# Kernel optimization log

Hardware: AMD Instinct MI355X
Metric: run time of the kernel (lower is better)

The kernel has to match this reference:

```python
import jax, jax.numpy as jnp
import numpy as np

DEGREE = 7

def setup_inputs() -> dict:
    key = jax.random.key(0)
    k1, k2 = jax.random.split(key)
    input_dims, output_dims = 1024, 1024
    x = jax.random.normal(k1, (8192, input_dims), dtype=jnp.float32)
    std = 1.0 / (input_dims * (DEGREE + 1))
    lucas_coeffs = std * jax.random.normal(k2, (input_dims, output_dims, DEGREE + 1), dtype=jnp.float32)
    return {"x": x, "lucas_coeffs": lucas_coeffs}

def reference(x, lucas_coeffs):
    input_dims = lucas_coeffs.shape[0]
    x = x.reshape(-1, input_dims)
    x = jnp.tanh(x)
    # Lucas polynomial recurrence: L0=2, L1=x, L_i = x*L_{i-1} + L_{i-2}
    basis = [jnp.full_like(x, 2.0)]
    if DEGREE > 0:
        basis.append(x)
    for i in range(2, DEGREE + 1):
        basis.append(x * basis[-1] + basis[-2])
    lucas = jnp.stack(basis, axis=-1)  # [b, i, d]
    y = jnp.einsum('bid,iod->bo', lucas, lucas_coeffs)
    return y
```

## Files before the change

kernel.cpp:

```cpp
#include <hip/hip_runtime.h>
#include <hip/hip_bf16.h>


typedef __attribute__((ext_vector_type(8)))  short  short8;
typedef __attribute__((ext_vector_type(4)))  unsigned short ushort4v;
typedef __attribute__((ext_vector_type(8)))  unsigned short ushort8;
typedef __attribute__((ext_vector_type(4)))  float  float4v;
typedef __attribute__((ext_vector_type(4)))  unsigned int uint4v;

#define M_DIM 8192
#define I_DIM 1024
#define O_DIM 1024
#define K_DIM 8192
#define BM 128
#define BN 128
#define BK 64
#define KSPLIT 2
#define KHALF (K_DIM / KSPLIT)
#define NSTEP (KHALF / BK)

__device__ __forceinline__ unsigned short f2bf(float f) {
    unsigned int u = __float_as_uint(f);
    u += 0x7FFFu + ((u >> 16) & 1u);
    return (unsigned short)(u >> 16);
}

__global__ __launch_bounds__(256) void zero_kernel(float* __restrict__ p) {
    int idx = (blockIdx.x * 256 + threadIdx.x) * 4;
    const float4v z = {0.f, 0.f, 0.f, 0.f};
    *(float4v*)(p + idx) = z;
}

__global__ __launch_bounds__(256) void prep_kernel(const float* __restrict__ x,
                                                   const float* __restrict__ c,
                                                   unsigned short* __restrict__ T,
                                                   unsigned short* __restrict__ Bt) {
    int bid = blockIdx.x;
    const int tPart = (M_DIM * I_DIM) / (8 * 256);
    if (bid < tPart) {
        int idx = (bid * 256 + threadIdx.x) * 8;
        float4v v0 = *(const float4v*)(x + idx);
        float4v v1 = *(const float4v*)(x + idx + 4);
        unsigned short t[8];
        t[0] = f2bf(tanhf(v0[0])); t[1] = f2bf(tanhf(v0[1]));
        t[2] = f2bf(tanhf(v0[2])); t[3] = f2bf(tanhf(v0[3]));
        t[4] = f2bf(tanhf(v1[0])); t[5] = f2bf(tanhf(v1[1]));
        t[6] = f2bf(tanhf(v1[2])); t[7] = f2bf(tanhf(v1[3]));
        ushort8 o;
        #pragma unroll
        for (int p = 0; p < 4; ++p) { o[2 * p] = t[p]; o[2 * p + 1] = t[p + 4]; }
        *(ushort8*)(T + idx) = o;
    } else {
        int idx = (bid - tPart) * 256 + threadIdx.x;
        int i = idx >> 10;
        int o = idx & 1023;
        const float* src = c + (size_t)i * 8192 + o * 8;
        float4v lo = *(const float4v*)(src);
        float4v hi = *(const float4v*)(src + 4);
        ushort8 v;
        v[0] = f2bf(lo[0]); v[1] = f2bf(lo[1]); v[2] = f2bf(lo[2]); v[3] = f2bf(lo[3]);
        v[4] = f2bf(hi[0]); v[5] = f2bf(hi[1]); v[6] = f2bf(hi[2]); v[7] = f2bf(hi[3]);
        *(ushort8*)(Bt + (size_t)o * K_DIM + i * 8) = v;
    }
}

__device__ __forceinline__ short8 lucas_frag(unsigned int tb) {
    const float t = __uint_as_float(tb << 16);
    const float L2v = fmaf(t, t, 2.0f);
    const float L3v = fmaf(t, L2v, t);
    const float L4v = fmaf(t, L3v, L2v);
    const float L5v = fmaf(t, L4v, L3v);
    const float L6v = fmaf(t, L5v, L4v);
    const float L7v = fmaf(t, L6v, L5v);
    union { uint4v u; short8 s; } r;
#if __has_builtin(__builtin_amdgcn_cvt_pk_bf16_f32)
    {
        auto p0 = __builtin_amdgcn_cvt_pk_bf16_f32(2.0f, t);
        auto p1 = __builtin_amdgcn_cvt_pk_bf16_f32(L2v, L3v);
        auto p2 = __builtin_amdgcn_cvt_pk_bf16_f32(L4v, L5v);
        auto p3 = __builtin_amdgcn_cvt_pk_bf16_f32(L6v, L7v);
        __builtin_memcpy(&r.u[0], &p0, 4);
        __builtin_memcpy(&r.u[1], &p1, 4);
        __builtin_memcpy(&r.u[2], &p2, 4);
        __builtin_memcpy(&r.u[3], &p3, 4);
    }
#else
    {
        r.u[0] = 0x4000u | (tb << 16);
        r.u[1] = __builtin_amdgcn_perm(__float_as_uint(L3v), __float_as_uint(L2v), 0x07060302);
        r.u[2] = __builtin_amdgcn_perm(__float_as_uint(L5v), __float_as_uint(L4v), 0x07060302);
        r.u[3] = __builtin_amdgcn_perm(__float_as_uint(L7v), __float_as_uint(L6v), 0x07060302);
    }
#endif
    return r.s;
}

__global__ __launch_bounds__(256, 4) void gemm_kernel(const unsigned short* __restrict__ T,
                                                      const unsigned short* __restrict__ Bt,
                                                      float* __restrict__ out) {
    __shared__ unsigned short Bs[2][BN * BK];
    __shared__ unsigned short Ts[2][BM * 8];

    const int tid  = threadIdx.x;
    const int lane = tid & 63;
    const int wave = tid >> 6;
    const int n0 = blockIdx.x * BN;
    const int m0 = blockIdx.y * BM;
    const int k0 = blockIdx.z * KHALF;

    const int wm0  = (wave >> 1) * 64;
    const int wn0  = (wave & 1) * 64;
    const int l16  = lane & 15;
    const int quad = lane >> 4;

    const int srow   = lane >> 3;
    const int il     = lane & 7;
    const int gchunk = il ^ srow;

    float4v acc[4][4];
    const float4v zero = {0.f, 0.f, 0.f, 0.f};
    #pragma unroll
    for (int a = 0; a < 4; ++a)
        #pragma unroll
        for (int b = 0; b < 4; ++b) acc[a][b] = zero;

    #pragma unroll
    for (int r = 0; r < 4; ++r) {
        const int rowb = r * 32 + wave * 8;
        const unsigned short* gB = Bt + (size_t)(n0 + rowb + srow) * K_DIM + k0 + gchunk * 8;
        __builtin_amdgcn_global_load_lds(
            (const __attribute__((address_space(1))) unsigned int*)gB,
            (__attribute__((address_space(3))) unsigned int*)&Bs[0][rowb * BK], 16, 0, 0);
    }
    if (wave < 2) {
        const unsigned short* gT = T + (size_t)(m0 + wave * 64 + lane) * I_DIM + k0 / 8;
        __builtin_amdgcn_global_load_lds(
            (const __attribute__((address_space(1))) unsigned int*)gT,
            (__attribute__((address_space(3))) unsigned int*)&Ts[0][wave * 64 * 8], 16, 0, 0);
    }
    __syncthreads();

    int cur = 0;
    for (int s = 0; s < NSTEP; ++s) {
        const int nxt = cur ^ 1;

        if (s + 1 < NSTEP) {
            const int kt = k0 + (s + 1) * BK;
            #pragma unroll
            for (int r = 0; r < 4; ++r) {
                const int rowb = r * 32 + wave * 8;
                const unsigned short* gB = Bt + (size_t)(n0 + rowb + srow) * K_DIM + kt + gchunk * 8;
                __builtin_amdgcn_global_load_lds(
                    (const __attribute__((address_space(1))) unsigned int*)gB,
                    (__attribute__((address_space(3))) unsigned int*)&Bs[nxt][rowb * BK], 16, 0, 0);
            }
            if (wave < 2) {
                const unsigned short* gT = T + (size_t)(m0 + wave * 64 + lane) * I_DIM + kt / 8;
                __builtin_amdgcn_global_load_lds(
                    (const __attribute__((address_space(1))) unsigned int*)gT,
                    (__attribute__((address_space(3))) unsigned int*)&Ts[nxt][wave * 64 * 8], 16, 0, 0);
            }
        }

        unsigned int tw[4];
        #pragma unroll
        for (int tt = 0; tt < 4; ++tt)
            tw[tt] = *(const unsigned int*)&Ts[cur][(wm0 + tt * 16 + l16) * 8 + quad * 2];

        #pragma unroll
        for (int k2 = 0; k2 < 2; ++k2) {
            short8 bfr[4];
            #pragma unroll
            for (int tn = 0; tn < 4; ++tn) {
                const int brow = wn0 + tn * 16 + l16;
                bfr[tn] = *(const short8*)&Bs[cur][brow * BK + (((k2 * 4 + quad) ^ (l16 & 7)) * 8)];
            }
            #pragma unroll
            for (int tt = 0; tt < 4; ++tt) {
                const short8 af = lucas_frag(k2 ? (tw[tt] >> 16) : (tw[tt] & 0xffffu));
                #pragma unroll
                for (int tn = 0; tn < 4; ++tn)
                    acc[tt][tn] = __builtin_amdgcn_mfma_f32_16x16x32_bf16(
                        af, bfr[tn], acc[tt][tn], 0, 0, 0);
            }
        }

        __syncthreads();
        cur = nxt;
    }

    #pragma unroll
    for (int tt = 0; tt < 4; ++tt) {
        #pragma unroll
        for (int tn = 0; tn < 4; ++tn) {
            const int col = n0 + wn0 + tn * 16 + l16;
            #pragma unroll
            for (int r = 0; r < 4; ++r) {
                const int row = m0 + wm0 + tt * 16 + quad * 4 + r;
                atomicAdd(&out[(size_t)row * O_DIM + col], acc[tt][tn][r]);
            }
        }
    }
}

__global__ __launch_bounds__(256) void naive_kernel(const float* __restrict__ x,
                                                    const float* __restrict__ c,
                                                    float* __restrict__ out) {
    int idx = blockIdx.x * 256 + threadIdx.x;
    int b = idx >> 10;
    int o = idx & 1023;
    const float* xb = x + (size_t)b * I_DIM;
    float acc = 0.f;
    for (int i = 0; i < I_DIM; ++i) {
        float t = tanhf(xb[i]);
        float L[8];
        L[0] = 2.0f; L[1] = t;
        #pragma unroll
        for (int d = 2; d < 8; ++d) L[d] = t * L[d - 1] + L[d - 2];
        const float* cc = c + (size_t)i * 8192 + o * 8;
        #pragma unroll
        for (int d = 0; d < 8; ++d) acc += L[d] * cc[d];
    }
    out[idx] = acc;
}

extern "C" void kernel_launch(void* const* d_in, const int* in_sizes, int n_in,
                              void* d_out, int out_size, void* d_ws, size_t ws_size,
                              hipStream_t stream) {
    const float* x      = (const float*)d_in[0];
    const float* coeffs = (const float*)d_in[1];
    float* out = (float*)d_out;

    const size_t btBytes = (size_t)O_DIM * K_DIM * sizeof(unsigned short);
    const size_t tBytes  = (size_t)M_DIM * I_DIM * sizeof(unsigned short);

    if (ws_size >= btBytes + tBytes) {
        unsigned short* Bt = (unsigned short*)d_ws;
        unsigned short* T  = (unsigned short*)((char*)d_ws + btBytes);

        zero_kernel<<<(M_DIM * O_DIM) / (4 * 256), 256, 0, stream>>>(out);

        const int tBlocks = (M_DIM * I_DIM) / (8 * 256);
        const int bBlocks = (I_DIM * O_DIM) / 256;
        prep_kernel<<<tBlocks + bBlocks, 256, 0, stream>>>(x, coeffs, T, Bt);

        dim3 grid(O_DIM / BN, M_DIM / BM, KSPLIT);
        gemm_kernel<<<grid, 256, 0, stream>>>(T, Bt, out);
    } else {
        naive_kernel<<<(M_DIM * O_DIM) / 256, 256, 0, stream>>>(x, coeffs, out);
    }
}
```

Before: 254.1 us.

## Use single-wave 128x128 GEMM blocks with manual waitcnt pipelining, no barriers

Restructures the GEMM so that each block is one 64-thread wave computing a full 128x128 output tile, with 8x8 MFMA accumulator fragments. This raises operand reuse per LDS fragment load. The block barriers are replaced by explicit s_waitcnt on vmcnt and lgkmcnt to double-buffer the global-to-LDS loads. In exchange, each SIMD has very few waves to hide latency, the wave issues all 18 async loads per stage itself, and holding 256 accumulator registers risks register pressure or spills.

```diff
diff --git a/kernel.cpp b/kernel.cpp
--- a/kernel.cpp
+++ b/kernel.cpp
@@ -12,12 +12,16 @@
 #define I_DIM 1024
 #define O_DIM 1024
 #define K_DIM 8192
-#define BM 128
-#define BN 128
+#define WM 128
+#define WN 128
 #define BK 64
 #define KSPLIT 2
 #define KHALF (K_DIM / KSPLIT)
 #define NSTEP (KHALF / BK)
+
+#define WAITCNT_VM18  0x4F72
+#define WAITCNT_VM0   0x0F70
+#define WAITCNT_LGKM0 0xC07F
 
 __device__ __forceinline__ unsigned short f2bf(float f) {
     unsigned int u = __float_as_uint(f);
@@ -95,108 +99,91 @@
     return r.s;
 }
 
-__global__ __launch_bounds__(256, 4) void gemm_kernel(const unsigned short* __restrict__ T,
-                                                      const unsigned short* __restrict__ Bt,
-                                                      float* __restrict__ out) {
-    __shared__ unsigned short Bs[2][BN * BK];
-    __shared__ unsigned short Ts[2][BM * 8];
-
-    const int tid  = threadIdx.x;
-    const int lane = tid & 63;
-    const int wave = tid >> 6;
-    const int n0 = blockIdx.x * BN;
-    const int m0 = blockIdx.y * BM;
+__global__ __launch_bounds__(64, 1) void gemm_kernel(const unsigned short* __restrict__ T,
+                                                     const unsigned short* __restrict__ Bt,
+                                                     float* __restrict__ out) {
+    __shared__ unsigned short Bs[2][WN * BK];
+    __shared__ unsigned short Ts[2][WM * 8];
+
+    const int lane = threadIdx.x;
+    const int n0 = blockIdx.x * WN;
+    const int m0 = blockIdx.y * WM;
     const int k0 = blockIdx.z * KHALF;
 
-    const int wm0  = (wave >> 1) * 64;
-    const int wn0  = (wave & 1) * 64;
     const int l16  = lane & 15;
     const int quad = lane >> 4;
-
-    const int srow   = lane >> 3;
-    const int il     = lane & 7;
+    const int srow = lane >> 3;
+    const int il   = lane & 7;
     const int gchunk = il ^ srow;
 
-    float4v acc[4][4];
+    float4v acc[8][8];
     const float4v zero = {0.f, 0.f, 0.f, 0.f};
     #pragma unroll
-    for (int a = 0; a < 4; ++a)
-        #pragma unroll
-        for (int b = 0; b < 4; ++b) acc[a][b] = zero;
-
-    #pragma unroll
-    for (int r = 0; r < 4; ++r) {
-        const int rowb = r * 32 + wave * 8;
-        const unsigned short* gB = Bt + (size_t)(n0 + rowb + srow) * K_DIM + k0 + gchunk * 8;
-        __builtin_amdgcn_global_load_lds(
-            (const __attribute__((address_space(1))) unsigned int*)gB,
-            (__attribute__((address_space(3))) unsigned int*)&Bs[0][rowb * BK], 16, 0, 0);
-    }
-    if (wave < 2) {
-        const unsigned short* gT = T + (size_t)(m0 + wave * 64 + lane) * I_DIM + k0 / 8;
-        __builtin_amdgcn_global_load_lds(
-            (const __attribute__((address_space(1))) unsigned int*)gT,
-            (__attribute__((address_space(3))) unsigned int*)&Ts[0][wave * 64 * 8], 16, 0, 0);
-    }
-    __syncthreads();
-
-    int cur = 0;
+    for (int a = 0; a < 8; ++a)
+        #pragma unroll
+        for (int b = 0; b < 8; ++b) acc[a][b] = zero;
+
+    auto stage = [&](int buf, int kt) {
+        #pragma unroll
+        for (int r = 0; r < 16; ++r) {
+            const unsigned short* gB = Bt + (size_t)(n0 + r * 8 + srow) * K_DIM + kt + gchunk * 8;
+            __builtin_amdgcn_global_load_lds(
+                (const __attribute__((address_space(1))) unsigned int*)gB,
+                (__attribute__((address_space(3))) unsigned int*)&Bs[buf][r * 8 * BK], 16, 0, 0);
+        }
+        #pragma unroll
+        for (int j = 0; j < 2; ++j) {
+            const unsigned short* gT = T + (size_t)(m0 + j * 64 + lane) * I_DIM + kt / 8;
+            __builtin_amdgcn_global_load_lds(
+                (const __attribute__((address_space(1))) unsigned int*)gT,
+                (__attribute__((address_space(3))) unsigned int*)&Ts[buf][j * 64 * 8], 16, 0, 0);
+        }
+    };
+
+    stage(0, k0);
+
     for (int s = 0; s < NSTEP; ++s) {
-        const int nxt = cur ^ 1;
-
+        const int cur = s & 1;
         if (s + 1 < NSTEP) {
-            const int kt = k0 + (s + 1) * BK;
+            __builtin_amdgcn_s_waitcnt(WAITCNT_LGKM0);
+            stage(cur ^ 1, k0 + (s + 1) * BK);
+            __builtin_amdgcn_s_waitcnt(WAITCNT_VM18);
+        } else {
+            __builtin_amdgcn_s_waitcnt(WAITCNT_VM0);
+        }
+
+        unsigned int tw[8];
+        #pragma unroll
+        for (int tt = 0; tt < 8; ++tt)
+            tw[tt] = *(const unsigned int*)&Ts[cur][(tt * 16 + l16) * 8 + quad * 2];
+
+        #pragma unroll
+        for (int k2 = 0; k2 < 2; ++k2) {
+            short8 bfr[8];
             #pragma unroll
-            for (int r = 0; r < 4; ++r) {
-                const int rowb = r * 32 + wave * 8;
-                const unsigned short* gB = Bt + (size_t)(n0 + rowb + srow) * K_DIM + kt + gchunk * 8;
-                __builtin_amdgcn_global_load_lds(
-                    (const __attribute__((address_space(1))) unsigned int*)gB,
-                    (__attribute__((address_space(3))) unsigned int*)&Bs[nxt][rowb * BK], 16, 0, 0);
-            }
-            if (wave < 2) {
-                const unsigned short* gT = T + (size_t)(m0 + wave * 64 + lane) * I_DIM + kt / 8;
-                __builtin_amdgcn_global_load_lds(
-                    (const __attribute__((address_space(1))) unsigned int*)gT,
-                    (__attribute__((address_space(3))) unsigned int*)&Ts[nxt][wave * 64 * 8], 16, 0, 0);
-            }
-        }
-
-        unsigned int tw[4];
-        #pragma unroll
-        for (int tt = 0; tt < 4; ++tt)
-            tw[tt] = *(const unsigned int*)&Ts[cur][(wm0 + tt * 16 + l16) * 8 + quad * 2];
-
-        #pragma unroll
-        for (int k2 = 0; k2 < 2; ++k2) {
-            short8 bfr[4];
-            #pragma unroll
-            for (int tn = 0; tn < 4; ++tn) {
-                const int brow = wn0 + tn * 16 + l16;
+            for (int tn = 0; tn < 8; ++tn) {
+                const int brow = tn * 16 + l16;
                 bfr[tn] = *(const short8*)&Bs[cur][brow * BK + (((k2 * 4 + quad) ^ (l16 & 7)) * 8)];
             }
             #pragma unroll
-            for (int tt = 0; tt < 4; ++tt) {
+            for (int tt = 0; tt < 8; ++tt) {
                 const short8 af = lucas_frag(k2 ? (tw[tt] >> 16) : (tw[tt] & 0xffffu));
                 #pragma unroll
-                for (int tn = 0; tn < 4; ++tn)
+                for (int tn = 0; tn < 8; ++tn)
                     acc[tt][tn] = __builtin_amdgcn_mfma_f32_16x16x32_bf16(
                         af, bfr[tn], acc[tt][tn], 0, 0, 0);
             }
         }
-
-        __syncthreads();
-        cur = nxt;
     }
 
     #pragma unroll
-    for (int tt = 0; tt < 4; ++tt) {
-        #pragma unroll
-        for (int tn = 0; tn < 4; ++tn) {
-            const int col = n0 + wn0 + tn * 16 + l16;
+    for (int tt = 0; tt < 8; ++tt) {
+        #pragma unroll
+        for (int tn = 0; tn < 8; ++tn) {
+            const int col = n0 + tn * 16 + l16;
             #pragma unroll
             for (int r = 0; r < 4; ++r) {
-                const int row = m0 + wm0 + tt * 16 + quad * 4 + r;
+                const int row = m0 + tt * 16 + quad * 4 + r;
                 atomicAdd(&out[(size_t)row * O_DIM + col], acc[tt][tn][r]);
             }
         }
@@ -244,8 +231,8 @@
         const int bBlocks = (I_DIM * O_DIM) / 256;
         prep_kernel<<<tBlocks + bBlocks, 256, 0, stream>>>(x, coeffs, T, Bt);
 
-        dim3 grid(O_DIM / BN, M_DIM / BM, KSPLIT);
-        gemm_kernel<<<grid, 256, 0, stream>>>(T, Bt, out);
+        dim3 grid(O_DIM / WN, M_DIM / WM, KSPLIT);
+        gemm_kernel<<<grid, 64, 0, stream>>>(T, Bt, out);
     } else {
         naive_kernel<<<(M_DIM * O_DIM) / 256, 256, 0, stream>>>(x, coeffs, out);
     }
```

Result: slower. 320.6 us (+26.2%).

## Switch GEMM to 32x32x16 MFMA with 256-row tiles and fuse zeroing into prep

Applied to the files above, without the earlier changes.

Switches the GEMM from 16x16x32 to 32x32x16 bf16 MFMA, with each wave owning 64 full rows by all 128 columns, and doubles the M tile to 256. The tanh prep kernel packs T differently so each lane reads 4 consecutive k-chunks in one 64-bit LDS load. The output-zeroing kernel is folded into the prep launch to save a launch. The larger tile and accumulator set raise register pressure, so launch bounds drop to 2 blocks per SIMD group, which lowers occupancy.

```diff
diff --git a/kernel.cpp b/kernel.cpp
--- a/kernel.cpp
+++ b/kernel.cpp
@@ -3,16 +3,16 @@
 
 
 typedef __attribute__((ext_vector_type(8)))  short  short8;
-typedef __attribute__((ext_vector_type(4)))  unsigned short ushort4v;
 typedef __attribute__((ext_vector_type(8)))  unsigned short ushort8;
 typedef __attribute__((ext_vector_type(4)))  float  float4v;
+typedef __attribute__((ext_vector_type(16))) float  float16v;
 typedef __attribute__((ext_vector_type(4)))  unsigned int uint4v;
 
 #define M_DIM 8192
 #define I_DIM 1024
 #define O_DIM 1024
 #define K_DIM 8192
-#define BM 128
+#define BM 256
 #define BN 128
 #define BK 64
 #define KSPLIT 2
@@ -25,20 +25,20 @@
     return (unsigned short)(u >> 16);
 }
 
-__global__ __launch_bounds__(256) void zero_kernel(float* __restrict__ p) {
-    int idx = (blockIdx.x * 256 + threadIdx.x) * 4;
-    const float4v z = {0.f, 0.f, 0.f, 0.f};
-    *(float4v*)(p + idx) = z;
-}
-
 __global__ __launch_bounds__(256) void prep_kernel(const float* __restrict__ x,
                                                    const float* __restrict__ c,
                                                    unsigned short* __restrict__ T,
-                                                   unsigned short* __restrict__ Bt) {
+                                                   unsigned short* __restrict__ Bt,
+                                                   float* __restrict__ outz) {
     int bid = blockIdx.x;
+    const int zPart = (M_DIM * O_DIM) / (4 * 256);
     const int tPart = (M_DIM * I_DIM) / (8 * 256);
-    if (bid < tPart) {
-        int idx = (bid * 256 + threadIdx.x) * 8;
+    if (bid < zPart) {
+        int idx = (bid * 256 + threadIdx.x) * 4;
+        const float4v z = {0.f, 0.f, 0.f, 0.f};
+        *(float4v*)(outz + idx) = z;
+    } else if (bid < zPart + tPart) {
+        int idx = ((bid - zPart) * 256 + threadIdx.x) * 8;
         float4v v0 = *(const float4v*)(x + idx);
         float4v v1 = *(const float4v*)(x + idx + 4);
         unsigned short t[8];
@@ -48,10 +48,10 @@
         t[6] = f2bf(tanhf(v1[2])); t[7] = f2bf(tanhf(v1[3]));
         ushort8 o;
         #pragma unroll
-        for (int p = 0; p < 4; ++p) { o[2 * p] = t[p]; o[2 * p + 1] = t[p + 4]; }
+        for (int p = 0; p < 4; ++p) { o[p] = t[2 * p]; o[4 + p] = t[2 * p + 1]; }
         *(ushort8*)(T + idx) = o;
     } else {
-        int idx = (bid - tPart) * 256 + threadIdx.x;
+        int idx = (bid - zPart - tPart) * 256 + threadIdx.x;
         int i = idx >> 10;
         int o = idx & 1023;
         const float* src = c + (size_t)i * 8192 + o * 8;
@@ -95,7 +95,7 @@
     return r.s;
 }
 
-__global__ __launch_bounds__(256, 4) void gemm_kernel(const unsigned short* __restrict__ T,
+__global__ __launch_bounds__(256, 2) void gemm_kernel(const unsigned short* __restrict__ T,
                                                       const unsigned short* __restrict__ Bt,
                                                       float* __restrict__ out) {
     __shared__ unsigned short Bs[2][BN * BK];
@@ -108,79 +108,64 @@
     const int m0 = blockIdx.y * BM;
     const int k0 = blockIdx.z * KHALF;
 
-    const int wm0  = (wave >> 1) * 64;
-    const int wn0  = (wave & 1) * 64;
-    const int l16  = lane & 15;
-    const int quad = lane >> 4;
+    const int l32 = lane & 31;
+    const int h   = lane >> 5;
+    const int wml = wave * 64;
 
     const int srow   = lane >> 3;
     const int il     = lane & 7;
     const int gchunk = il ^ srow;
 
-    float4v acc[4][4];
-    const float4v zero = {0.f, 0.f, 0.f, 0.f};
+    float16v acc[2][4];
     #pragma unroll
-    for (int a = 0; a < 4; ++a)
-        #pragma unroll
-        for (int b = 0; b < 4; ++b) acc[a][b] = zero;
-
-    #pragma unroll
-    for (int r = 0; r < 4; ++r) {
-        const int rowb = r * 32 + wave * 8;
-        const unsigned short* gB = Bt + (size_t)(n0 + rowb + srow) * K_DIM + k0 + gchunk * 8;
-        __builtin_amdgcn_global_load_lds(
-            (const __attribute__((address_space(1))) unsigned int*)gB,
-            (__attribute__((address_space(3))) unsigned int*)&Bs[0][rowb * BK], 16, 0, 0);
-    }
-    if (wave < 2) {
-        const unsigned short* gT = T + (size_t)(m0 + wave * 64 + lane) * I_DIM + k0 / 8;
+    for (int a = 0; a < 2; ++a)
+        #pragma unroll
+        for (int b = 0; b < 4; ++b)
+            #pragma unroll
+            for (int e = 0; e < 16; ++e) acc[a][b][e] = 0.f;
+
+    auto stage = [&](int buf, int kt) {
+        #pragma unroll
+        for (int r = 0; r < 4; ++r) {
+            const int rowb = r * 32 + wave * 8;
+            const unsigned short* gB = Bt + (size_t)(n0 + rowb + srow) * K_DIM + kt + gchunk * 8;
+            __builtin_amdgcn_global_load_lds(
+                (const __attribute__((address_space(1))) unsigned int*)gB,
+                (__attribute__((address_space(3))) unsigned int*)&Bs[buf][rowb * BK], 16, 0, 0);
+        }
+        const unsigned short* gT = T + (size_t)(m0 + wml + lane) * I_DIM + kt / 8;
         __builtin_amdgcn_global_load_lds(
             (const __attribute__((address_space(1))) unsigned int*)gT,
-            (__attribute__((address_space(3))) unsigned int*)&Ts[0][wave * 64 * 8], 16, 0, 0);
-    }
+            (__attribute__((address_space(3))) unsigned int*)&Ts[buf][wml * 8], 16, 0, 0);
+    };
+
+    stage(0, k0);
     __syncthreads();
 
     int cur = 0;
     for (int s = 0; s < NSTEP; ++s) {
         const int nxt = cur ^ 1;
-
-        if (s + 1 < NSTEP) {
-            const int kt = k0 + (s + 1) * BK;
-            #pragma unroll
-            for (int r = 0; r < 4; ++r) {
-                const int rowb = r * 32 + wave * 8;
-                const unsigned short* gB = Bt + (size_t)(n0 + rowb + srow) * K_DIM + kt + gchunk * 8;
-                __builtin_amdgcn_global_load_lds(
-                    (const __attribute__((address_space(1))) unsigned int*)gB,
-                    (__attribute__((address_space(3))) unsigned int*)&Bs[nxt][rowb * BK], 16, 0, 0);
+        if (s + 1 < NSTEP) stage(nxt, k0 + (s + 1) * BK);
+
+        unsigned long long tw[2];
+        #pragma unroll
+        for (int tt = 0; tt < 2; ++tt)
+            tw[tt] = *(const unsigned long long*)&Ts[cur][(wml + tt * 32 + l32) * 8 + h * 4];
+
+        #pragma unroll
+        for (int kk = 0; kk < 4; ++kk) {
+            short8 bfr[4];
+            #pragma unroll
+            for (int tn = 0; tn < 4; ++tn) {
+                const int brow = tn * 32 + l32;
+                bfr[tn] = *(const short8*)&Bs[cur][brow * BK + (((kk * 2 + h) ^ (brow & 7)) * 8)];
             }
-            if (wave < 2) {
-                const unsigned short* gT = T + (size_t)(m0 + wave * 64 + lane) * I_DIM + kt / 8;
-                __builtin_amdgcn_global_load_lds(
-                    (const __attribute__((address_space(1))) unsigned int*)gT,
-                    (__attribute__((address_space(3))) unsigned int*)&Ts[nxt][wave * 64 * 8], 16, 0, 0);
-            }
-        }
-
-        unsigned int tw[4];
-        #pragma unroll
-        for (int tt = 0; tt < 4; ++tt)
-            tw[tt] = *(const unsigned int*)&Ts[cur][(wm0 + tt * 16 + l16) * 8 + quad * 2];
-
-        #pragma unroll
-        for (int k2 = 0; k2 < 2; ++k2) {
-            short8 bfr[4];
-            #pragma unroll
-            for (int tn = 0; tn < 4; ++tn) {
-                const int brow = wn0 + tn * 16 + l16;
-                bfr[tn] = *(const short8*)&Bs[cur][brow * BK + (((k2 * 4 + quad) ^ (l16 & 7)) * 8)];
-            }
-            #pragma unroll
-            for (int tt = 0; tt < 4; ++tt) {
-                const short8 af = lucas_frag(k2 ? (tw[tt] >> 16) : (tw[tt] & 0xffffu));
+            #pragma unroll
+            for (int tt = 0; tt < 2; ++tt) {
+                const short8 af = lucas_frag((unsigned int)((tw[tt] >> (16 * kk)) & 0xffffu));
                 #pragma unroll
                 for (int tn = 0; tn < 4; ++tn)
-                    acc[tt][tn] = __builtin_amdgcn_mfma_f32_16x16x32_bf16(
+                    acc[tt][tn] = __builtin_amdgcn_mfma_f32_32x32x16_bf16(
                         af, bfr[tn], acc[tt][tn], 0, 0, 0);
             }
         }
@@ -190,14 +175,14 @@
     }
 
     #pragma unroll
-    for (int tt = 0; tt < 4; ++tt) {
+    for (int tt = 0; tt < 2; ++tt) {
         #pragma unroll
         for (int tn = 0; tn < 4; ++tn) {
-            const int col = n0 + wn0 + tn * 16 + l16;
-            #pragma unroll
-            for (int r = 0; r < 4; ++r) {
-                const int row = m0 + wm0 + tt * 16 + quad * 4 + r;
-                atomicAdd(&out[(size_t)row * O_DIM + col], acc[tt][tn][r]);
+            const int col = n0 + tn * 32 + l32;
+            #pragma unroll
+            for (int reg = 0; reg < 16; ++reg) {
+                const int row = m0 + wml + tt * 32 + (reg & 3) + 8 * (reg >> 2) + 4 * h;
+                atomicAdd(&out[(size_t)row * O_DIM + col], acc[tt][tn][reg]);
             }
         }
     }
@@ -238,11 +223,10 @@
         unsigned short* Bt = (unsigned short*)d_ws;
         unsigned short* T  = (unsigned short*)((char*)d_ws + btBytes);
 
-        zero_kernel<<<(M_DIM * O_DIM) / (4 * 256), 256, 0, stream>>>(out);
-
+        const int zBlocks = (M_DIM * O_DIM) / (4 * 256);
         const int tBlocks = (M_DIM * I_DIM) / (8 * 256);
         const int bBlocks = (I_DIM * O_DIM) / 256;
-        prep_kernel<<<tBlocks + bBlocks, 256, 0, stream>>>(x, coeffs, T, Bt);
+        prep_kernel<<<zBlocks + tBlocks + bBlocks, 256, 0, stream>>>(x, coeffs, T, Bt, out);
 
         dim3 grid(O_DIM / BN, M_DIM / BM, KSPLIT);
         gemm_kernel<<<grid, 256, 0, stream>>>(T, Bt, out);
```

Measured after the change: 259.9 us. 1.02x slower.
